# Performance work log

Measured on AMD Instinct MI355X. Metric: run time of the kernel, lower is better.

The kernel has to match this reference:

```python
import jax, jax.numpy as jnp
import numpy as np

jax.config.update("jax_enable_x64", True)

B, S = 256, 256
TINY = float(np.finfo(np.float64).tiny)  # torch.finfo().tiny for double


def _matrix_tree_logZ(scores, mask):
    """scores: [B,S,S] float64, mask: [B,S] bool (col 0 is False).
    Returns sum over batch of log partition function (Matrix-Tree theorem)."""
    lens = mask.sum(-1)  # token counts per sentence (excludes root col)
    mask_r = mask.at[:, 0].set(True)  # index_fill(1, 0, 1)
    pair = mask_r[:, :, None] & mask_r[:, None, :]  # [B,S,S]
    s = jnp.where(pair, scores, -jnp.inf)
    m = jnp.max(s.reshape(s.shape[0], -1), axis=-1)  # [B] per-batch max for stability
    A = jnp.maximum(jnp.exp(s - m[:, None, None]), TINY)  # clamp like torch
    idx = jnp.arange(S)
    D = jnp.zeros_like(A).at[:, idx, idx].set(A.sum(-1))  # degree matrix
    eye = jnp.eye(S, dtype=A.dtype)
    # masked_scatter_: rows with mask_r True take (D - A) rows, else identity
    L = jnp.where(mask_r[:, :, None], D - A, eye)
    logZ = jnp.linalg.slogdet(L[:, 1:, 1:])[1] + m * lens
    return logZ.sum()


def setup_inputs() -> dict:
    key = jax.random.key(0)
    k1, k2 = jax.random.split(key)
    scores = jax.random.normal(k1, (B, S, S), dtype=jnp.float32)
    lens = jax.random.randint(k2, (B,), S // 2, S)  # sentence lengths
    pos = jnp.arange(S)
    # col 0 (pseudo root) False, padding beyond length False
    mask = (pos[None, :] >= 1) & (pos[None, :] < lens[:, None])
    return {"scores": scores, "mask": mask}


def reference(scores, mask):
    # mbr=True path: marginals = d logZ / d scores (computed in double like torch)
    s64 = scores.astype(jnp.float64)
    probs = jax.grad(_matrix_tree_logZ)(s64, mask)
    return probs.astype(jnp.float32)
```

## Files before the change

kernel.cpp:

```cpp
#include <hip/hip_runtime.h>
#include <math.h>


#define S 256
#define BB 256

__device__ __forceinline__ int rowmap(int lr, int kb) {
    int rt = lr >> 6;
    int rb = rt + (rt >= kb ? 1 : 0);
    return rb * 64 + (lr & 63);
}

__global__ __launch_bounds__(256) void k_max(const float* __restrict__ sc,
                                             float* __restrict__ partial) {
    int b = blockIdx.y, rg = blockIdx.x;
    const float4* p4 = (const float4*)(sc + (size_t)b * S * S + rg * 8192);
    int tid = threadIdx.x;
    float4 v[8];
    #pragma unroll
    for (int it = 0; it < 8; ++it) v[it] = p4[tid + 256 * it];
    float m = -1e30f;
    #pragma unroll
    for (int it = 0; it < 8; ++it)
        m = fmaxf(m, fmaxf(fmaxf(v[it].x, v[it].y), fmaxf(v[it].z, v[it].w)));
    for (int off = 32; off > 0; off >>= 1) m = fmaxf(m, __shfl_down(m, off));
    __shared__ float sm[4];
    if ((tid & 63) == 0) sm[tid >> 6] = m;
    __syncthreads();
    if (tid == 0) partial[b * 8 + rg] = fmaxf(fmaxf(sm[0], sm[1]), fmaxf(sm[2], sm[3]));
}

__global__ void k_n(const unsigned char* __restrict__ mk, const float* __restrict__ partial,
                    double* __restrict__ mb, int* __restrict__ nb) {
    int b = blockIdx.x, j = threadIdx.x;
    __shared__ int shc[4];

    const unsigned int* mw = (const unsigned int*)mk;
    unsigned int w0 = mw[0], w1 = mw[1];
    int mode = (w0 != 0u) ? 0 : ((w1 != 0u) ? 1 : 2);

    int c;
    if (mode == 0)      c = (mk[(size_t)b * S + j] != 0);
    else if (mode == 1) c = (((const int*)mk)[(size_t)b * S + j] != 0);
    else                c = (((const long long*)mk)[(size_t)b * S + j] != 0LL);

    int lane = j & 63, wid = j >> 6;
    int cs = c;
    for (int off = 32; off > 0; off >>= 1) cs += __shfl_down(cs, off);
    if (lane == 0) shc[wid] = cs;
    __syncthreads();
    if (j == 0) {
        nb[b] = shc[0] + shc[1] + shc[2] + shc[3];
        float mm = partial[b * 8];
        #pragma unroll
        for (int q = 1; q < 8; ++q) mm = fmaxf(mm, partial[b * 8 + q]);
        mb[b] = (double)mm;
    }
}

__global__ __launch_bounds__(256) void k_build(const float* __restrict__ sc,
                                               const double* __restrict__ mb,
                                               const int* __restrict__ nb,
                                               double* __restrict__ Mg) {
    int b = blockIdx.y;
    int wid = threadIdx.x >> 6, lane = threadIdx.x & 63;
    int p = blockIdx.x * 4 + wid;
    int n = nb[b];
    double m = mb[b];
    __shared__ double se[4][260];
    double* Mrow = Mg + ((size_t)b * S + p) * S;
    bool act = (p < n);
    double ssum = 0.0;
    #pragma unroll
    for (int c4 = 0; c4 < 4; ++c4) {
        int j = lane + 64 * c4;
        double ev = 0.0;
        if (act && j <= n)
            ev = (double)expf((float)((double)sc[((size_t)b * S + (p + 1)) * S + j] - m));
        se[wid][j] = ev;
        ssum += ev;
    }
    for (int off = 32; off > 0; off >>= 1) ssum += __shfl_down(ssum, off);
    ssum = __shfl(ssum, 0);
    __syncthreads();
    #pragma unroll
    for (int c4 = 0; c4 < 4; ++c4) {
        int j = lane + 64 * c4;
        double v;
        if (act && j < n) v = ((j == p) ? ssum : 0.0) - se[wid][j + 1];
        else              v = (j == p) ? 1.0 : 0.0;
        Mrow[j] = v;
    }
}

__global__ __launch_bounds__(256) void k_gjrow(double* __restrict__ Mg, double* __restrict__ Pg,
                                               int kb) {
    int b = blockIdx.x, tid = threadIdx.x;
    double* M = Mg + (size_t)b * S * S;
    double* P = Pg + (size_t)b * 4096;
    __shared__ double PT[64][66];
    __shared__ double Rs[64][200];
    __shared__ double rbuf[2][64];
    __shared__ double cbuf[2][64];

    int i = tid >> 2, g = tid & 3, c0 = g << 4;
    double c[16];
    #pragma unroll
    for (int u = 0; u < 16; ++u)
        c[u] = M[(size_t)(kb * 64 + i) * S + kb * 64 + c0 + u];

    if (i == 0) {
        #pragma unroll
        for (int u = 0; u < 16; ++u) rbuf[0][c0 + u] = c[u];
    }
    if (g == 0) cbuf[0][i] = c[0];

    for (int kt = 0; kt < 4; ++kt) {
        #pragma unroll
        for (int ks = 0; ks < 16; ++ks) {
            int k = kt * 16 + ks;
            const int par = ks & 1;
            __syncthreads();
            double pv = rbuf[par][k];
            double f  = cbuf[par][i];
            double rk[16];
            #pragma unroll
            for (int m2 = 0; m2 < 8; ++m2) {
                double2 t = *(const double2*)&rbuf[par][c0 + 2 * m2];
                rk[2 * m2] = t.x; rk[2 * m2 + 1] = t.y;
            }
            double pivinv = 1.0 / pv;
            if (i == k) {
                #pragma unroll
                for (int u = 0; u < 16; ++u)
                    c[u] = ((g == kt) && (u == ks)) ? pivinv : c[u] * pivinv;
            } else {
                double gm = f * pivinv;
                #pragma unroll
                for (int u = 0; u < 16; ++u)
                    c[u] = ((g == kt) && (u == ks)) ? (-gm) : fma(-gm, rk[u], c[u]);
            }
            if (i == k + 1) {
                #pragma unroll
                for (int u = 0; u < 16; ++u) rbuf[par ^ 1][c0 + u] = c[u];
            }
            if (ks < 15) { if (g == kt)     cbuf[par ^ 1][i] = c[ks + 1]; }
            else         { if (g == kt + 1) cbuf[par ^ 1][i] = c[0]; }
        }
    }
    #pragma unroll
    for (int u = 0; u < 16; ++u) {
        PT[c0 + u][i] = c[u];
        P[i * 64 + c0 + u] = c[u];
        M[(size_t)(kb * 64 + i) * S + kb * 64 + c0 + u] = c[u];
    }
    {
        int cidx = tid & 63;
        #pragma unroll
        for (int rep = 0; rep < 16; ++rep) {
            int r = rep * 4 + (tid >> 6);
            #pragma unroll
            for (int cc = 0; cc < 3; ++cc) {
                int j = cc * 64 + cidx;
                Rs[r][j] = M[(size_t)(kb * 64 + r) * S + rowmap(j, kb)];
            }
        }
    }
    __syncthreads();

    int tx = tid & 15, ty = tid >> 4;
    double2 acc[4][6];
    #pragma unroll
    for (int q = 0; q < 4; ++q)
        #pragma unroll
        for (int w = 0; w < 6; ++w) acc[q][w] = double2{0.0, 0.0};

    for (int s = 0; s < 64; ++s) {
        double2 p01 = *(const double2*)&PT[s][4 * ty];
        double2 p23 = *(const double2*)&PT[s][4 * ty + 2];
        #pragma unroll
        for (int w = 0; w < 6; ++w) {
            double2 r = *(const double2*)&Rs[s][2 * tx + 32 * w];
            acc[0][w].x = fma(p01.x, r.x, acc[0][w].x); acc[0][w].y = fma(p01.x, r.y, acc[0][w].y);
            acc[1][w].x = fma(p01.y, r.x, acc[1][w].x); acc[1][w].y = fma(p01.y, r.y, acc[1][w].y);
            acc[2][w].x = fma(p23.x, r.x, acc[2][w].x); acc[2][w].y = fma(p23.x, r.y, acc[2][w].y);
            acc[3][w].x = fma(p23.y, r.x, acc[3][w].x); acc[3][w].y = fma(p23.y, r.y, acc[3][w].y);
        }
    }
    #pragma unroll
    for (int q = 0; q < 4; ++q) {
        size_t row = (size_t)(kb * 64 + 4 * ty + q) * S;
        #pragma unroll
        for (int w = 0; w < 6; ++w) {
            int j = 2 * tx + 32 * w;
            *(double2*)&M[row + rowmap(j, kb)] = acc[q][w];
        }
    }
}

__global__ __launch_bounds__(256) void k_int(double* __restrict__ Mg, int kb) {
    int id = blockIdx.x;
    int b = id >> 1, half = id & 1;
    double* M = Mg + (size_t)b * S * S;
    int tid = threadIdx.x;
    __shared__ double FTs[32][98];
    __shared__ double Rss[32][200];

    int tx = tid & 15, ty = tid >> 4;
    double2 acc[6][6];
    #pragma unroll
    for (int q = 0; q < 6; ++q)
        #pragma unroll
        for (int w = 0; w < 6; ++w) acc[q][w] = double2{0.0, 0.0};

    for (int ck = 0; ck < 2; ++ck) {
        __syncthreads();
        {
            int kk = tid & 31, lrb = (tid >> 5) * 12;
            #pragma unroll
            for (int q = 0; q < 12; ++q) {
                int lrg = half * 96 + lrb + q;
                FTs[kk][lrb + q] =
                    M[(size_t)rowmap(lrg, kb) * S + kb * 64 + ck * 32 + kk];
            }
            int jl = tid & 63, ss = tid >> 6;
            #pragma unroll
            for (int rep = 0; rep < 8; ++rep) {
                int kk2 = ss + 4 * rep;
                #pragma unroll
                for (int cc = 0; cc < 3; ++cc) {
                    int j = cc * 64 + jl;
                    Rss[kk2][j] = M[(size_t)(kb * 64 + ck * 32 + kk2) * S + rowmap(j, kb)];
                }
            }
        }
        __syncthreads();
        for (int kk = 0; kk < 32; ++kk) {
            double2 f01 = *(const double2*)&FTs[kk][6 * ty];
            double2 f23 = *(const double2*)&FTs[kk][6 * ty + 2];
            double2 f45 = *(const double2*)&FTs[kk][6 * ty + 4];
            #pragma unroll
            for (int w = 0; w < 6; ++w) {
                double2 r = *(const double2*)&Rss[kk][2 * tx + 32 * w];
                acc[0][w].x = fma(f01.x, r.x, acc[0][w].x); acc[0][w].y = fma(f01.x, r.y, acc[0][w].y);
                acc[1][w].x = fma(f01.y, r.x, acc[1][w].x); acc[1][w].y = fma(f01.y, r.y, acc[1][w].y);
                acc[2][w].x = fma(f23.x, r.x, acc[2][w].x); acc[2][w].y = fma(f23.x, r.y, acc[2][w].y);
                acc[3][w].x = fma(f23.y, r.x, acc[3][w].x); acc[3][w].y = fma(f23.y, r.y, acc[3][w].y);
                acc[4][w].x = fma(f45.x, r.x, acc[4][w].x); acc[4][w].y = fma(f45.x, r.y, acc[4][w].y);
                acc[5][w].x = fma(f45.y, r.x, acc[5][w].x); acc[5][w].y = fma(f45.y, r.y, acc[5][w].y);
            }
        }
    }
    #pragma unroll
    for (int q = 0; q < 6; ++q) {
        int lrg = half * 96 + ty * 6 + q;
        size_t row = (size_t)rowmap(lrg, kb) * S;
        #pragma unroll
        for (int w = 0; w < 6; ++w) {
            int j = 2 * tx + 32 * w;
            double* p = &M[row + rowmap(j, kb)];
            double2 old = *(double2*)p;
            *(double2*)p = double2{old.x - acc[q][w].x, old.y - acc[q][w].y};
        }
    }
}

__global__ __launch_bounds__(256) void k_colP(double* __restrict__ Mg,
                                              const double* __restrict__ Pg, int kb) {
    int id = blockIdx.x;
    int b = id >> 1, half = id & 1;
    double* M = Mg + (size_t)b * S * S;
    const double* P = Pg + (size_t)b * 4096;
    int tid = threadIdx.x;
    __shared__ double FTs[32][98];
    __shared__ double Ps[32][66];

    int tx = tid & 15, ty = tid >> 4;
    double2 acc[6][2];
    #pragma unroll
    for (int q = 0; q < 6; ++q) { acc[q][0] = double2{0.0, 0.0}; acc[q][1] = double2{0.0, 0.0}; }

    for (int ck = 0; ck < 2; ++ck) {
        __syncthreads();
        {
            int kk = tid & 31, lrb = (tid >> 5) * 12;
            #pragma unroll
            for (int q = 0; q < 12; ++q) {
                int lrg = half * 96 + lrb + q;
                FTs[kk][lrb + q] =
                    M[(size_t)rowmap(lrg, kb) * S + kb * 64 + ck * 32 + kk];
            }
            int u = tid & 63;
            #pragma unroll
            for (int rep = 0; rep < 8; ++rep) {
                int r = rep * 4 + (tid >> 6);
                Ps[r][u] = P[(ck * 32 + r) * 64 + u];
            }
        }
        __syncthreads();
        for (int kk = 0; kk < 32; ++kk) {
            double2 f01 = *(const double2*)&FTs[kk][6 * ty];
            double2 f23 = *(const double2*)&FTs[kk][6 * ty + 2];
            double2 f45 = *(const double2*)&FTs[kk][6 * ty + 4];
            #pragma unroll
            for (int w = 0; w < 2; ++w) {
                double2 r = *(const double2*)&Ps[kk][2 * tx + 32 * w];
                acc[0][w].x = fma(f01.x, r.x, acc[0][w].x); acc[0][w].y = fma(f01.x, r.y, acc[0][w].y);
                acc[1][w].x = fma(f01.y, r.x, acc[1][w].x); acc[1][w].y = fma(f01.y, r.y, acc[1][w].y);
                acc[2][w].x = fma(f23.x, r.x, acc[2][w].x); acc[2][w].y = fma(f23.x, r.y, acc[2][w].y);
                acc[3][w].x = fma(f23.y, r.x, acc[3][w].x); acc[3][w].y = fma(f23.y, r.y, acc[3][w].y);
                acc[4][w].x = fma(f45.x, r.x, acc[4][w].x); acc[4][w].y = fma(f45.x, r.y, acc[4][w].y);
                acc[5][w].x = fma(f45.y, r.x, acc[5][w].x); acc[5][w].y = fma(f45.y, r.y, acc[5][w].y);
            }
        }
    }
    #pragma unroll
    for (int q = 0; q < 6; ++q) {
        int lrg = half * 96 + ty * 6 + q;
        size_t row = (size_t)rowmap(lrg, kb) * S + kb * 64;
        #pragma unroll
        for (int w = 0; w < 2; ++w) {
            int u = 2 * tx + 32 * w;
            *(double2*)&M[row + u] = double2{-acc[q][w].x, -acc[q][w].y};
        }
    }
}

__global__ __launch_bounds__(256) void k_xt(const double* __restrict__ Mg,
                                            float* __restrict__ outF,
                                            double* __restrict__ Dg) {
    int b = blockIdx.y, t = blockIdx.x;
    int r = t & 3, c = t >> 2;
    const double* M = Mg + (size_t)b * S * S;
    __shared__ float L[64][65];
    int tid = threadIdx.x;
    int cc = tid & 63;
    #pragma unroll
    for (int rep = 0; rep < 16; ++rep) {
        int rr = rep * 4 + (tid >> 6);
        L[rr][cc] = (float)M[(size_t)(64 * r + rr) * S + 64 * c + cc];
    }
    if (r == c && tid < 64)
        Dg[(size_t)b * S + 64 * r + tid] = M[(size_t)(64 * r + tid) * S + 64 * r + tid];
    __syncthreads();
    int pp = tid & 63;
    #pragma unroll
    for (int rep = 0; rep < 16; ++rep) {
        int qq = rep * 4 + (tid >> 6);
        int orow = 64 * c + qq + 1, ocol = 64 * r + pp + 1;
        if (orow < 256 && ocol < 256)
            outF[((size_t)b * S + orow) * S + ocol] = L[pp][qq];
    }
}

__global__ __launch_bounds__(256) void k_epi2(const float* __restrict__ sc,
                                              const double* __restrict__ Dg,
                                              const double* __restrict__ mb,
                                              const int* __restrict__ nb,
                                              float* __restrict__ out) {
    int b = blockIdx.y;
    int idx4 = blockIdx.x * 256 + threadIdx.x;
    int i = idx4 >> 6;
    int jq = idx4 & 63;
    int n = nb[b];
    float m = (float)mb[b];
    size_t base = ((size_t)b * S + i) * S + 4 * jq;
    float4 xf = *(const float4*)(out + base);
    float4 s4 = *(const float4*)(sc + base);
    double dg = (i >= 1) ? Dg[(size_t)b * S + i - 1] : 0.0;
    float xfa[4] = {xf.x, xf.y, xf.z, xf.w};
    float sa[4]  = {s4.x, s4.y, s4.z, s4.w};
    float ra[4];
    #pragma unroll
    for (int comp = 0; comp < 4; ++comp) {
        int j = 4 * jq + comp;
        float v = 0.0f;
        if (i >= 1 && i <= n && j <= n) {
            double A = (double)expf(sa[comp] - m);
            double sub = (j >= 1) ? (double)xfa[comp] : 0.0;
            v = (float)(A * (dg - sub));
        }
        ra[comp] = v;
    }
    *(float4*)(out + base) = float4{ra[0], ra[1], ra[2], ra[3]};
}

extern "C" void kernel_launch(void* const* d_in, const int* in_sizes, int n_in,
                              void* d_out, int out_size, void* d_ws, size_t ws_size,
                              hipStream_t stream) {
    (void)in_sizes; (void)n_in; (void)out_size; (void)ws_size;
    const float* sc = (const float*)d_in[0];
    const unsigned char* mk = (const unsigned char*)d_in[1];
    double* ws = (double*)d_ws;

    double* M  = ws;
    double* P  = M + (size_t)BB * S * S;
    double* mb = P + (size_t)BB * 4096;
    int*    nb = (int*)(mb + BB);
    double* Dg = mb + 2 * BB;
    float*  partial = (float*)P;
    float*  out = (float*)d_out;

    k_max<<<dim3(8, BB), 256, 0, stream>>>(sc, partial);
    k_n<<<BB, 256, 0, stream>>>(mk, partial, mb, nb);
    k_build<<<dim3(64, BB), 256, 0, stream>>>(sc, mb, nb, M);
    for (int kb = 0; kb < 4; ++kb) {
        k_gjrow<<<BB, 256, 0, stream>>>(M, P, kb);
        k_int<<<2 * BB, 256, 0, stream>>>(M, kb);
        k_colP<<<2 * BB, 256, 0, stream>>>(M, P, kb);
    }
    k_xt<<<dim3(16, BB), 256, 0, stream>>>(M, out, Dg);
    k_epi2<<<dim3(64, BB), 256, 0, stream>>>(sc, Dg, mb, nb, out);
}
```

Baseline: 600.6 us.

## Fuse interior and column-panel updates into one Gauss-Jordan update kernel

Replaces the separate k_int and k_colP launches with a single k_upd kernel per batch (512 threads) that treats the full pivot row block, including the pivot column written by k_gjrow, as one 16x256 panel. For the pivot column it overwrites with the negated product, and for the other columns it subtracts. This removes one launch per block step and the redundant reloads of the F panel. k_gjrow also prefetches its R panel into registers before the elimination loop so the global loads overlap with the pivot work. The cost is fewer blocks (256 instead of 512), a sequential loop over the two row halves, and about 48 more registers per thread in k_gjrow.

```diff
diff --git a/kernel.cpp b/kernel.cpp
--- a/kernel.cpp
+++ b/kernel.cpp
@@ -109,6 +109,20 @@
     for (int u = 0; u < 16; ++u)
         c[u] = M[(size_t)(kb * 64 + i) * S + kb * 64 + c0 + u];
 
+    double rst[48];
+    {
+        int cidx = tid & 63;
+        #pragma unroll
+        for (int rep = 0; rep < 16; ++rep) {
+            int r = rep * 4 + (tid >> 6);
+            #pragma unroll
+            for (int cc = 0; cc < 3; ++cc) {
+                int j = cc * 64 + cidx;
+                rst[rep * 3 + cc] = M[(size_t)(kb * 64 + r) * S + rowmap(j, kb)];
+            }
+        }
+    }
+
     if (i == 0) {
         #pragma unroll
         for (int u = 0; u < 16; ++u) rbuf[0][c0 + u] = c[u];
@@ -160,10 +174,8 @@
         for (int rep = 0; rep < 16; ++rep) {
             int r = rep * 4 + (tid >> 6);
             #pragma unroll
-            for (int cc = 0; cc < 3; ++cc) {
-                int j = cc * 64 + cidx;
-                Rs[r][j] = M[(size_t)(kb * 64 + r) * S + rowmap(j, kb)];
-            }
+            for (int cc = 0; cc < 3; ++cc)
+                Rs[r][cc * 64 + cidx] = rst[rep * 3 + cc];
         }
     }
     __syncthreads();
@@ -198,130 +210,65 @@
     }
 }
 
-__global__ __launch_bounds__(256) void k_int(double* __restrict__ Mg, int kb) {
-    int id = blockIdx.x;
-    int b = id >> 1, half = id & 1;
+__global__ __launch_bounds__(512) void k_upd(double* __restrict__ Mg, int kb) {
+    int b = blockIdx.x;
     double* M = Mg + (size_t)b * S * S;
     int tid = threadIdx.x;
-    __shared__ double FTs[32][98];
-    __shared__ double Rss[32][200];
-
-    int tx = tid & 15, ty = tid >> 4;
-    double2 acc[6][6];
-    #pragma unroll
-    for (int q = 0; q < 6; ++q)
-        #pragma unroll
-        for (int w = 0; w < 6; ++w) acc[q][w] = double2{0.0, 0.0};
-
-    for (int ck = 0; ck < 2; ++ck) {
-        __syncthreads();
-        {
-            int kk = tid & 31, lrb = (tid >> 5) * 12;
-            #pragma unroll
-            for (int q = 0; q < 12; ++q) {
-                int lrg = half * 96 + lrb + q;
-                FTs[kk][lrb + q] =
-                    M[(size_t)rowmap(lrg, kb) * S + kb * 64 + ck * 32 + kk];
-            }
-            int jl = tid & 63, ss = tid >> 6;
+    __shared__ double Hs[16][258];
+    __shared__ double FTs[16][98];
+    int tx = tid & 31, ty = tid >> 5;
+
+    for (int half = 0; half < 2; ++half) {
+        double2 acc[6][4];
+        #pragma unroll
+        for (int q = 0; q < 6; ++q)
+            #pragma unroll
+            for (int w = 0; w < 4; ++w) acc[q][w] = double2{0.0, 0.0};
+
+        for (int ck = 0; ck < 4; ++ck) {
+            __syncthreads();
             #pragma unroll
             for (int rep = 0; rep < 8; ++rep) {
-                int kk2 = ss + 4 * rep;
+                int idx = rep * 512 + tid;
+                int kk = idx >> 8, col = idx & 255;
+                Hs[kk][col] = M[(size_t)(kb * 64 + ck * 16 + kk) * S + col];
+            }
+            #pragma unroll
+            for (int rep = 0; rep < 3; ++rep) {
+                int idx = rep * 512 + tid;
+                int kk = idx & 15, lr = idx >> 4;
+                FTs[kk][lr] = M[(size_t)rowmap(half * 96 + lr, kb) * S + kb * 64 + ck * 16 + kk];
+            }
+            __syncthreads();
+            for (int kk = 0; kk < 16; ++kk) {
+                double2 f01 = *(const double2*)&FTs[kk][6 * ty];
+                double2 f23 = *(const double2*)&FTs[kk][6 * ty + 2];
+                double2 f45 = *(const double2*)&FTs[kk][6 * ty + 4];
                 #pragma unroll
-                for (int cc = 0; cc < 3; ++cc) {
-                    int j = cc * 64 + jl;
-                    Rss[kk2][j] = M[(size_t)(kb * 64 + ck * 32 + kk2) * S + rowmap(j, kb)];
+                for (int w = 0; w < 4; ++w) {
+                    double2 h = *(const double2*)&Hs[kk][2 * tx + 64 * w];
+                    acc[0][w].x = fma(f01.x, h.x, acc[0][w].x); acc[0][w].y = fma(f01.x, h.y, acc[0][w].y);
+                    acc[1][w].x = fma(f01.y, h.x, acc[1][w].x); acc[1][w].y = fma(f01.y, h.y, acc[1][w].y);
+                    acc[2][w].x = fma(f23.x, h.x, acc[2][w].x); acc[2][w].y = fma(f23.x, h.y, acc[2][w].y);
+                    acc[3][w].x = fma(f23.y, h.x, acc[3][w].x); acc[3][w].y = fma(f23.y, h.y, acc[3][w].y);
+                    acc[4][w].x = fma(f45.x, h.x, acc[4][w].x); acc[4][w].y = fma(f45.x, h.y, acc[4][w].y);
+                    acc[5][w].x = fma(f45.y, h.x, acc[5][w].x); acc[5][w].y = fma(f45.y, h.y, acc[5][w].y);
                 }
             }
         }
-        __syncthreads();
-        for (int kk = 0; kk < 32; ++kk) {
-            double2 f01 = *(const double2*)&FTs[kk][6 * ty];
-            double2 f23 = *(const double2*)&FTs[kk][6 * ty + 2];
-            double2 f45 = *(const double2*)&FTs[kk][6 * ty + 4];
-            #pragma unroll
-            for (int w = 0; w < 6; ++w) {
-                double2 r = *(const double2*)&Rss[kk][2 * tx + 32 * w];
-                acc[0][w].x = fma(f01.x, r.x, acc[0][w].x); acc[0][w].y = fma(f01.x, r.y, acc[0][w].y);
-                acc[1][w].x = fma(f01.y, r.x, acc[1][w].x); acc[1][w].y = fma(f01.y, r.y, acc[1][w].y);
-                acc[2][w].x = fma(f23.x, r.x, acc[2][w].x); acc[2][w].y = fma(f23.x, r.y, acc[2][w].y);
-                acc[3][w].x = fma(f23.y, r.x, acc[3][w].x); acc[3][w].y = fma(f23.y, r.y, acc[3][w].y);
-                acc[4][w].x = fma(f45.x, r.x, acc[4][w].x); acc[4][w].y = fma(f45.x, r.y, acc[4][w].y);
-                acc[5][w].x = fma(f45.y, r.x, acc[5][w].x); acc[5][w].y = fma(f45.y, r.y, acc[5][w].y);
-            }
-        }
-    }
-    #pragma unroll
-    for (int q = 0; q < 6; ++q) {
-        int lrg = half * 96 + ty * 6 + q;
-        size_t row = (size_t)rowmap(lrg, kb) * S;
-        #pragma unroll
-        for (int w = 0; w < 6; ++w) {
-            int j = 2 * tx + 32 * w;
-            double* p = &M[row + rowmap(j, kb)];
-            double2 old = *(double2*)p;
-            *(double2*)p = double2{old.x - acc[q][w].x, old.y - acc[q][w].y};
-        }
-    }
-}
-
-__global__ __launch_bounds__(256) void k_colP(double* __restrict__ Mg,
-                                              const double* __restrict__ Pg, int kb) {
-    int id = blockIdx.x;
-    int b = id >> 1, half = id & 1;
-    double* M = Mg + (size_t)b * S * S;
-    const double* P = Pg + (size_t)b * 4096;
-    int tid = threadIdx.x;
-    __shared__ double FTs[32][98];
-    __shared__ double Ps[32][66];
-
-    int tx = tid & 15, ty = tid >> 4;
-    double2 acc[6][2];
-    #pragma unroll
-    for (int q = 0; q < 6; ++q) { acc[q][0] = double2{0.0, 0.0}; acc[q][1] = double2{0.0, 0.0}; }
-
-    for (int ck = 0; ck < 2; ++ck) {
-        __syncthreads();
-        {
-            int kk = tid & 31, lrb = (tid >> 5) * 12;
-            #pragma unroll
-            for (int q = 0; q < 12; ++q) {
-                int lrg = half * 96 + lrb + q;
-                FTs[kk][lrb + q] =
-                    M[(size_t)rowmap(lrg, kb) * S + kb * 64 + ck * 32 + kk];
-            }
-            int u = tid & 63;
-            #pragma unroll
-            for (int rep = 0; rep < 8; ++rep) {
-                int r = rep * 4 + (tid >> 6);
-                Ps[r][u] = P[(ck * 32 + r) * 64 + u];
-            }
-        }
-        __syncthreads();
-        for (int kk = 0; kk < 32; ++kk) {
-            double2 f01 = *(const double2*)&FTs[kk][6 * ty];
-            double2 f23 = *(const double2*)&FTs[kk][6 * ty + 2];
-            double2 f45 = *(const double2*)&FTs[kk][6 * ty + 4];
-            #pragma unroll
-            for (int w = 0; w < 2; ++w) {
-                double2 r = *(const double2*)&Ps[kk][2 * tx + 32 * w];
-                acc[0][w].x = fma(f01.x, r.x, acc[0][w].x); acc[0][w].y = fma(f01.x, r.y, acc[0][w].y);
-                acc[1][w].x = fma(f01.y, r.x, acc[1][w].x); acc[1][w].y = fma(f01.y, r.y, acc[1][w].y);
-                acc[2][w].x = fma(f23.x, r.x, acc[2][w].x); acc[2][w].y = fma(f23.x, r.y, acc[2][w].y);
-                acc[3][w].x = fma(f23.y, r.x, acc[3][w].x); acc[3][w].y = fma(f23.y, r.y, acc[3][w].y);
-                acc[4][w].x = fma(f45.x, r.x, acc[4][w].x); acc[4][w].y = fma(f45.x, r.y, acc[4][w].y);
-                acc[5][w].x = fma(f45.y, r.x, acc[5][w].x); acc[5][w].y = fma(f45.y, r.y, acc[5][w].y);
-            }
-        }
-    }
-    #pragma unroll
-    for (int q = 0; q < 6; ++q) {
-        int lrg = half * 96 + ty * 6 + q;
-        size_t row = (size_t)rowmap(lrg, kb) * S + kb * 64;
-        #pragma unroll
-        for (int w = 0; w < 2; ++w) {
-            int u = 2 * tx + 32 * w;
-            *(double2*)&M[row + u] = double2{-acc[q][w].x, -acc[q][w].y};
+        #pragma unroll
+        for (int q = 0; q < 6; ++q) {
+            size_t row = (size_t)rowmap(half * 96 + ty * 6 + q, kb) * S;
+            #pragma unroll
+            for (int w = 0; w < 4; ++w) {
+                int j0 = 2 * tx + 64 * w;
+                if (w == kb) {
+                    *(double2*)&M[row + j0] = double2{-acc[q][w].x, -acc[q][w].y};
+                } else {
+                    double2 old = *(const double2*)&M[row + j0];
+                    *(double2*)&M[row + j0] = double2{old.x - acc[q][w].x, old.y - acc[q][w].y};
+                }
+            }
         }
     }
 }
@@ -406,8 +353,7 @@
     k_build<<<dim3(64, BB), 256, 0, stream>>>(sc, mb, nb, M);
     for (int kb = 0; kb < 4; ++kb) {
         k_gjrow<<<BB, 256, 0, stream>>>(M, P, kb);
-        k_int<<<2 * BB, 256, 0, stream>>>(M, kb);
-        k_colP<<<2 * BB, 256, 0, stream>>>(M, P, kb);
+        k_upd<<<BB, 512, 0, stream>>>(M, kb);
     }
     k_xt<<<dim3(16, BB), 256, 0, stream>>>(M, out, Dg);
     k_epi2<<<dim3(64, BB), 256, 0, stream>>>(sc, Dg, mb, nb, out);
```

After: 639.3 us. 1.06x slower.
